# Kernel tuning notes

Hardware: AMD Instinct MI355X
Metric: run time of the kernel (lower is better)

Reference implementation:

```python
import jax, jax.numpy as jnp
import numpy as np


def setup_inputs() -> dict:
    key = jax.random.key(0)
    ks = jax.random.split(key, 12)
    N, D = 150000, 100          # user_num + news_num nodes, emb_dim
    T, E, S = 16, 262144, 4096  # timesteps, edges/step, seeds/step
    CAT, K = 20, 9
    return {
        "node_emb": jax.random.normal(ks[0], (N, D), jnp.float32),
        "cx": jax.random.normal(ks[1], (N, D), jnp.float32),
        "rel_emb": jax.random.normal(ks[2], (CAT, D), jnp.float32),
        "W_ih": jax.random.normal(ks[3], (4 * D, D), jnp.float32) * 0.1,
        "W_hh": jax.random.normal(ks[4], (4 * D, D), jnp.float32) * 0.1,
        "b_ih": jax.random.normal(ks[5], (4 * D,), jnp.float32) * 0.1,
        "b_hh": jax.random.normal(ks[6], (4 * D,), jnp.float32) * 0.1,
        "src": jax.random.randint(ks[7], (T, E), 0, N, jnp.int64),
        "dst": jax.random.randint(ks[8], (T, E), 0, N, jnp.int64),
        "cat": jax.random.randint(ks[9], (T, E), 0, CAT, jnp.int64),
        "seeds": jax.random.randint(ks[10], (T, S), 0, 100000, jnp.int64),
        "cand_idx": jax.random.randint(ks[11], (T * S, K), 0, N, jnp.int64),
    }


def reference(node_emb, cx, rel_emb, W_ih, W_hh, b_ih, b_hh,
              src, dst, cat, seeds, cand_idx):
    N, D = node_emb.shape

    def step(carry, inputs):
        emb, c = carry
        s, d, ct, seed = inputs
        # previous hidden/cell state of seed users (before aggregation)
        h_prev = emb[seed]            # [S, D]
        c_prev = c[seed]              # [S, D]
        # edge-weighted gather-multiply-mean aggregation (send_and_recv)
        msg = emb[s] * rel_emb[ct]    # [E, D]
        agg = jax.ops.segment_sum(msg, d, num_segments=N)          # [N, D]
        cnt = jax.ops.segment_sum(jnp.ones(d.shape, emb.dtype), d,
                                  num_segments=N)                  # [N]
        emb = emb + agg / jnp.maximum(cnt, 1.0)[:, None]           # residual add
        # LSTMCell update on seed users
        x = emb[seed]                                              # [S, D]
        gates = x @ W_ih.T + b_ih + h_prev @ W_hh.T + b_hh         # [S, 4D]
        i_g, f_g, g_g, o_g = jnp.split(gates, 4, axis=-1)
        c_new = jax.nn.sigmoid(f_g) * c_prev + jax.nn.sigmoid(i_g) * jnp.tanh(g_g)
        h_new = jax.nn.sigmoid(o_g) * jnp.tanh(c_new)
        emb = emb.at[seed].set(h_new)
        c = c.at[seed].set(c_new)
        return (emb, c), h_new

    (emb_final, _), seed_embs = jax.lax.scan(
        step, (node_emb, cx), (src, dst, cat, seeds))
    # seed_embs: [T, S, D] -> per-click user embeddings
    user = seed_embs.reshape(-1, D)           # [T*S, D]
    cand = emb_final[cand_idx]                # [T*S, K, D]
    scores = jnp.einsum('nd,nkd->nk', user, cand)
    return scores
```

## Files before the change

### kernel.cpp

```cpp
#include <hip/hip_runtime.h>
#include <math.h>

#define N_NODES 150000
#define NODE_STRIDE 150016
#define DIM 100
#define D4 25
#define T_STEPS 16
#define E_EDGES 262144
#define S_SEEDS 4096
#define K_CAND 9
#define SPB 16
#define NPB 8

#define CB 32
#define BSPAN 4688

__device__ __forceinline__ float sigmoidf_(float x) {
    return 1.0f / (1.0f + __expf(-x));
}


__global__ __launch_bounds__(256) void coarse_hist(
    const int* __restrict__ dst, int* __restrict__ ccnt) {
    int t = blockIdx.x >> 10;
    int i = blockIdx.x * 256 + threadIdx.x;
    __shared__ int h[CB];
    if (threadIdx.x < CB) h[threadIdx.x] = 0;
    __syncthreads();
    int d = dst[i];
    atomicAdd(&h[d / BSPAN], 1);
    __syncthreads();
    if (threadIdx.x < CB)
        atomicAdd(&ccnt[t * CB + threadIdx.x], h[threadIdx.x]);
}

__global__ __launch_bounds__(64) void coarse_scan(
    const int* __restrict__ ccnt, int* __restrict__ coffs,
    int* __restrict__ ccur) {
    int t = blockIdx.x;
    int tid = threadIdx.x;
    __shared__ int sh[CB];
    if (tid < CB) sh[tid] = ccnt[t * CB + tid];
    __syncthreads();
    if (tid == 0) {
        int run = 0;
        for (int b = 0; b < CB; b++) { int c = sh[b]; sh[b] = run; run += c; }
    }
    __syncthreads();
    if (tid < CB) {
        coffs[t * (CB + 1) + tid] = sh[tid];
        ccur[t * CB + tid] = sh[tid];
    }
    if (tid == 0) coffs[t * (CB + 1) + CB] = E_EDGES;
}

__global__ __launch_bounds__(256) void coarse_scatter(
    const int* __restrict__ src, const int* __restrict__ dst,
    const int* __restrict__ cat, int* __restrict__ ccur,
    int2* __restrict__ cbuf) {
    int t = blockIdx.x >> 10;
    int i = blockIdx.x * 256 + threadIdx.x;
    __shared__ int h[CB];
    __shared__ int base[CB];
    if (threadIdx.x < CB) h[threadIdx.x] = 0;
    __syncthreads();
    int d = dst[i];
    int b = d / BSPAN;
    int rank = atomicAdd(&h[b], 1);
    __syncthreads();
    if (threadIdx.x < CB && h[threadIdx.x] > 0)
        base[threadIdx.x] = atomicAdd(&ccur[t * CB + threadIdx.x], h[threadIdx.x]);
    __syncthreads();
    int2 entry;
    entry.x = src[i] | (cat[i] << 18);
    entry.y = d;
    cbuf[(size_t)t * E_EDGES + base[b] + rank] = entry;
}

__global__ __launch_bounds__(256) void fine_build(
    const int2* __restrict__ cbuf, const int* __restrict__ coffs,
    int4* __restrict__ meta, int* __restrict__ sorted) {
    int t = blockIdx.x >> 5;
    int b = blockIdx.x & 31;
    int node0 = b * BSPAN;
    int nodes = min(BSPAN, N_NODES - node0);
    int ebeg = coffs[t * (CB + 1) + b];
    int eend = coffs[t * (CB + 1) + b + 1];
    const int2* ebuf = cbuf + (size_t)t * E_EDGES;
    int4* mt = meta + (size_t)t * NODE_STRIDE;
    int* srt = sorted + (size_t)t * E_EDGES;
    __shared__ int cnt[BSPAN];
    __shared__ int begs[BSPAN];
    __shared__ int sums[256];
    int tid = threadIdx.x;

    for (int j = tid; j < BSPAN; j += 256) cnt[j] = 0;
    __syncthreads();
    for (int e = ebeg + tid; e < eend; e += 256)
        atomicAdd(&cnt[ebuf[e].y - node0], 1);
    __syncthreads();

    const int chunk = (BSPAN + 255) / 256;
    int cbeg = tid * chunk;
    int cend = min(cbeg + chunk, BSPAN);
    int s = 0;
    for (int j = cbeg; j < cend; j++) s += cnt[j];
    sums[tid] = s;
    __syncthreads();
    for (int d = 1; d < 256; d <<= 1) {
        int v = (tid >= d) ? sums[tid - d] : 0;
        __syncthreads();
        sums[tid] += v;
        __syncthreads();
    }
    int run = (tid == 0) ? 0 : sums[tid - 1];
    for (int j = cbeg; j < cend; j++) {
        int c = cnt[j];
        begs[j] = run;
        cnt[j] = run;
        run += c;
    }
    __syncthreads();

    for (int e = ebeg + tid; e < eend; e += 256) {
        int2 en = ebuf[e];
        int pos = atomicAdd(&cnt[en.y - node0], 1);
        srt[ebeg + pos] = en.x;
    }
    __syncthreads();

    for (int j = tid; j < nodes; j += 256) {
        int lbeg = begs[j];
        int deg = cnt[j] - lbeg;
        int gbeg = ebeg + lbeg;
        int4 m;
        m.x = deg;
        m.y = gbeg;
        m.z = (deg > 0) ? srt[gbeg] : 0;
        m.w = (deg > 1) ? srt[gbeg + 1] : 0;
        mt[node0 + j] = m;
    }
}

__global__ __launch_bounds__(256) void fused_agg(
    const float* __restrict__ emb_in, float* __restrict__ emb_out,
    const float* __restrict__ rel_emb, const int4* __restrict__ meta,
    const int* __restrict__ sorted) {
    int g = threadIdx.x >> 5;
    int lane = threadIdx.x & 31;
    int node = blockIdx.x * NPB + g;
    if (node >= N_NODES) return;
    bool act = lane < D4;
    int4 m = meta[node];
    int deg = m.x;
    float4 own = act ? ((const float4*)(emb_in + (size_t)node * DIM))[lane]
                     : make_float4(0.f, 0.f, 0.f, 0.f);
    float4 acc = make_float4(0.f, 0.f, 0.f, 0.f);
    if (deg > 0 && act) {
        float4 m0 = ((const float4*)(emb_in + (size_t)(m.z & 0x3FFFF) * DIM))[lane];
        float4 r0 = ((const float4*)(rel_emb + (size_t)(m.z >> 18) * DIM))[lane];
        float4 m1, r1;
        if (deg > 1) {
            m1 = ((const float4*)(emb_in + (size_t)(m.w & 0x3FFFF) * DIM))[lane];
            r1 = ((const float4*)(rel_emb + (size_t)(m.w >> 18) * DIM))[lane];
        }
        acc.x += m0.x * r0.x; acc.y += m0.y * r0.y;
        acc.z += m0.z * r0.z; acc.w += m0.w * r0.w;
        if (deg > 1) {
            acc.x += m1.x * r1.x; acc.y += m1.y * r1.y;
            acc.z += m1.z * r1.z; acc.w += m1.w * r1.w;
        }
    }
    for (int e = m.y + 2; e < m.y + deg; e++) {
        int p = sorted[e];
        if (act) {
            float4 mm = ((const float4*)(emb_in + (size_t)(p & 0x3FFFF) * DIM))[lane];
            float4 rr = ((const float4*)(rel_emb + (size_t)(p >> 18) * DIM))[lane];
            acc.x += mm.x * rr.x; acc.y += mm.y * rr.y;
            acc.z += mm.z * rr.z; acc.w += mm.w * rr.w;
        }
    }
    if (act) {
        float inv = (deg > 0) ? 1.0f / (float)deg : 0.0f;
        own.x += acc.x * inv; own.y += acc.y * inv;
        own.z += acc.z * inv; own.w += acc.w * inv;
        ((float4*)(emb_out + (size_t)node * DIM))[lane] = own;
    }
}

__global__ __launch_bounds__(512) void lstm_kernel(
    const float* __restrict__ emb_new, const float* __restrict__ emb_old,
    const float* __restrict__ c_state, const int* __restrict__ seeds,
    const float* __restrict__ W_ih, const float* __restrict__ W_hh,
    const float* __restrict__ b_ih, const float* __restrict__ b_hh,
    float* __restrict__ h_out, float* __restrict__ c_out) {
    __shared__ __align__(16) float xs[SPB][DIM];
    __shared__ __align__(16) float hs[SPB][DIM];
    __shared__ float gates[SPB][4 * DIM];
    int tid = threadIdx.x;
    int base = blockIdx.x * SPB;

    for (int idx = tid; idx < SPB * DIM; idx += 512) {
        int s = idx / DIM, d = idx - s * DIM;
        int node = seeds[base + s];
        xs[s][d] = emb_new[(size_t)node * DIM + d];
        hs[s][d] = emb_old[(size_t)node * DIM + d];
    }
    __syncthreads();

    if (tid < 4 * DIM) {
        int j = tid;
        float acc[SPB];
#pragma unroll
        for (int s = 0; s < SPB; s++) acc[s] = 0.0f;
        const float4* wi = (const float4*)(W_ih + (size_t)j * DIM);
        const float4* wh = (const float4*)(W_hh + (size_t)j * DIM);
        for (int dc = 0; dc < D4; dc++) {
            float4 a = wi[dc], b = wh[dc];
#pragma unroll
            for (int s = 0; s < SPB; s++) {
                float4 x = ((const float4*)xs[s])[dc];
                float4 h = ((const float4*)hs[s])[dc];
                acc[s] += x.x * a.x + x.y * a.y + x.z * a.z + x.w * a.w
                        + h.x * b.x + h.y * b.y + h.z * b.z + h.w * b.w;
            }
        }
        float bb = b_ih[j] + b_hh[j];
#pragma unroll
        for (int s = 0; s < SPB; s++) gates[s][j] = acc[s] + bb;
    }
    __syncthreads();

    for (int idx = tid; idx < SPB * DIM; idx += 512) {
        int s = idx / DIM, d = idx - s * DIM;
        int node = seeds[base + s];
        float ig = gates[s][d];
        float fg = gates[s][DIM + d];
        float gg = gates[s][2 * DIM + d];
        float og = gates[s][3 * DIM + d];
        float cp = c_state[(size_t)node * DIM + d];
        float cn = sigmoidf_(fg) * cp + sigmoidf_(ig) * tanhf(gg);
        float hn = sigmoidf_(og) * tanhf(cn);
        h_out[(size_t)(base + s) * DIM + d] = hn;
        c_out[(size_t)(base + s) * DIM + d] = cn;
    }
}

__global__ __launch_bounds__(256) void scatter_seed(
    float* __restrict__ emb, float* __restrict__ c_state,
    const int* __restrict__ seeds,
    const float* __restrict__ h_new, const float* __restrict__ c_new) {
    int i = blockIdx.x * blockDim.x + threadIdx.x;
    int sd = i / D4, q = i - sd * D4;
    int node = seeds[sd];
    ((float4*)(emb + (size_t)node * DIM))[q] =
        ((const float4*)(h_new + (size_t)sd * DIM))[q];
    ((float4*)(c_state + (size_t)node * DIM))[q] =
        ((const float4*)(c_new + (size_t)sd * DIM))[q];
}

__global__ __launch_bounds__(64) void score_kernel(
    const float* __restrict__ seed_h, const float* __restrict__ emb,
    const int* __restrict__ cand_idx, float* __restrict__ out) {
    int n = blockIdx.x;
    int lane = threadIdx.x;
    float u0 = seed_h[(size_t)n * DIM + lane];
    float u1 = (lane + 64 < DIM) ? seed_h[(size_t)n * DIM + lane + 64] : 0.0f;
    for (int k = 0; k < K_CAND; k++) {
        int node = cand_idx[n * K_CAND + k];
        const float* ce = emb + (size_t)node * DIM;
        float p = u0 * ce[lane];
        if (lane + 64 < DIM) p += u1 * ce[lane + 64];
        for (int off = 32; off > 0; off >>= 1) p += __shfl_down(p, off);
        if (lane == 0) out[n * K_CAND + k] = p;
    }
}

extern "C" void kernel_launch(void* const* d_in, const int* in_sizes, int n_in,
                              void* d_out, int out_size, void* d_ws, size_t ws_size,
                              hipStream_t stream) {
    const float* node_emb = (const float*)d_in[0];
    const float* cx       = (const float*)d_in[1];
    const float* rel_emb  = (const float*)d_in[2];
    const float* W_ih     = (const float*)d_in[3];
    const float* W_hh     = (const float*)d_in[4];
    const float* b_ih     = (const float*)d_in[5];
    const float* b_hh     = (const float*)d_in[6];
    const int*   src      = (const int*)d_in[7];
    const int*   dst      = (const int*)d_in[8];
    const int*   cat      = (const int*)d_in[9];
    const int*   seeds    = (const int*)d_in[10];
    const int*   cand     = (const int*)d_in[11];
    float* out = (float*)d_out;

    char* wsb = (char*)d_ws;
    float* emb_a = (float*)wsb; wsb += sizeof(float) * (size_t)N_NODES * DIM;
    float* emb_b = (float*)wsb; wsb += sizeof(float) * (size_t)N_NODES * DIM;
    float* cst   = (float*)wsb; wsb += sizeof(float) * (size_t)N_NODES * DIM;
    float* cnew  = (float*)wsb; wsb += sizeof(float) * (size_t)S_SEEDS * DIM;
    float* seedh = (float*)wsb; wsb += sizeof(float) * (size_t)T_STEPS * S_SEEDS * DIM;
    int4* meta   = (int4*)wsb; wsb += sizeof(int4) * (size_t)T_STEPS * NODE_STRIDE;
    int* sorted  = (int*)wsb; wsb += sizeof(int) * (size_t)T_STEPS * E_EDGES;
    int* ccnt    = (int*)wsb; wsb += sizeof(int) * T_STEPS * CB;
    int* ccur    = (int*)wsb; wsb += sizeof(int) * T_STEPS * CB;
    int* coffs   = (int*)wsb; wsb += sizeof(int) * T_STEPS * (CB + 1);
    int2* cbuf = (int2*)emb_b;

    hipMemsetAsync(ccnt, 0, sizeof(int) * T_STEPS * CB, stream);
    coarse_hist<<<T_STEPS * 1024, 256, 0, stream>>>(dst, ccnt);
    coarse_scan<<<T_STEPS, 64, 0, stream>>>(ccnt, coffs, ccur);
    coarse_scatter<<<T_STEPS * 1024, 256, 0, stream>>>(src, dst, cat, ccur, cbuf);
    fine_build<<<T_STEPS * CB, 256, 0, stream>>>(cbuf, coffs, meta, sorted);

    hipMemcpyAsync(emb_a, node_emb, sizeof(float) * (size_t)N_NODES * DIM,
                   hipMemcpyDeviceToDevice, stream);
    hipMemcpyAsync(cst, cx, sizeof(float) * (size_t)N_NODES * DIM,
                   hipMemcpyDeviceToDevice, stream);

    float* cur = emb_a;
    float* nxt = emb_b;
    for (int t = 0; t < T_STEPS; t++) {
        fused_agg<<<(N_NODES + NPB - 1) / NPB, 256, 0, stream>>>(
            cur, nxt, rel_emb,
            meta + (size_t)t * NODE_STRIDE, sorted + (size_t)t * E_EDGES);
        lstm_kernel<<<S_SEEDS / SPB, 512, 0, stream>>>(
            nxt, cur, cst, seeds + (size_t)t * S_SEEDS,
            W_ih, W_hh, b_ih, b_hh,
            seedh + (size_t)t * S_SEEDS * DIM, cnew);
        scatter_seed<<<(S_SEEDS * D4) / 256, 256, 0, stream>>>(
            nxt, cst, seeds + (size_t)t * S_SEEDS,
            seedh + (size_t)t * S_SEEDS * DIM, cnew);
        float* tmp = cur; cur = nxt; nxt = tmp;
    }
    score_kernel<<<T_STEPS * S_SEEDS, 64, 0, stream>>>(seedh, cur, cand, out);
}
```

Baseline: 1.690 ms.

## Use per-block histograms for edge bucketing, inline third neighbor, skip embedding copy

Coarse edge bucketing now computes per-block histograms and scans them, replacing global atomic cursors, with 64 buckets and 8 edges per thread. Node metadata packs degree and begin offset into one word so a third neighbor index can be stored inline, avoiding a dependent load from the sorted array for low-degree nodes. The initial device copy of node_emb is removed by reading the input directly at step 0 and alternating output buffers. This adds a serial per-column scan and depends on degrees fitting in 13 bits.

```diff
diff --git a/kernel.cpp b/kernel.cpp
--- a/kernel.cpp
+++ b/kernel.cpp
@@ -12,8 +12,11 @@
 #define SPB 16
 #define NPB 8
 
-#define CB 32
-#define BSPAN 4688
+#define CB 64
+#define BSPAN 2344
+#define EPT 8
+#define EPB (256 * EPT)
+#define CBLK (E_EDGES / EPB)
 
 __device__ __forceinline__ float sigmoidf_(float x) {
     return 1.0f / (1.0f + __expf(-x));
@@ -21,67 +24,85 @@
 
 
 __global__ __launch_bounds__(256) void coarse_hist(
-    const int* __restrict__ dst, int* __restrict__ ccnt) {
-    int t = blockIdx.x >> 10;
-    int i = blockIdx.x * 256 + threadIdx.x;
+    const int* __restrict__ dst, int* __restrict__ bh) {
+    int t = blockIdx.x / CBLK;
+    int blk = blockIdx.x % CBLK;
+    int base = t * E_EDGES + blk * EPB;
+    int tid = threadIdx.x;
     __shared__ int h[CB];
-    if (threadIdx.x < CB) h[threadIdx.x] = 0;
-    __syncthreads();
-    int d = dst[i];
-    atomicAdd(&h[d / BSPAN], 1);
-    __syncthreads();
-    if (threadIdx.x < CB)
-        atomicAdd(&ccnt[t * CB + threadIdx.x], h[threadIdx.x]);
-}
-
-__global__ __launch_bounds__(64) void coarse_scan(
-    const int* __restrict__ ccnt, int* __restrict__ coffs,
-    int* __restrict__ ccur) {
+    if (tid < CB) h[tid] = 0;
+    __syncthreads();
+#pragma unroll
+    for (int e = 0; e < EPT; e++) {
+        int d = dst[base + e * 256 + tid];
+        atomicAdd(&h[d / BSPAN], 1);
+    }
+    __syncthreads();
+    if (tid < CB) bh[(t * CBLK + blk) * CB + tid] = h[tid];
+}
+
+__global__ __launch_bounds__(64) void scan_bh(
+    int* __restrict__ bh, int* __restrict__ coffs) {
     int t = blockIdx.x;
-    int tid = threadIdx.x;
-    __shared__ int sh[CB];
-    if (tid < CB) sh[tid] = ccnt[t * CB + tid];
-    __syncthreads();
-    if (tid == 0) {
-        int run = 0;
-        for (int b = 0; b < CB; b++) { int c = sh[b]; sh[b] = run; run += c; }
-    }
-    __syncthreads();
-    if (tid < CB) {
-        coffs[t * (CB + 1) + tid] = sh[tid];
-        ccur[t * CB + tid] = sh[tid];
-    }
-    if (tid == 0) coffs[t * (CB + 1) + CB] = E_EDGES;
+    int b = threadIdx.x;
+    int run = 0;
+    for (int blk = 0; blk < CBLK; blk++) {
+        int idx = (t * CBLK + blk) * CB + b;
+        int v = bh[idx];
+        bh[idx] = run;
+        run += v;
+    }
+    __shared__ int tot[CB];
+    tot[b] = run;
+    __syncthreads();
+    if (b == 0) {
+        int r = 0;
+        for (int i = 0; i < CB; i++) { int c = tot[i]; tot[i] = r; r += c; }
+    }
+    __syncthreads();
+    coffs[t * (CB + 1) + b] = tot[b];
+    if (b == 0) coffs[t * (CB + 1) + CB] = E_EDGES;
 }
 
 __global__ __launch_bounds__(256) void coarse_scatter(
     const int* __restrict__ src, const int* __restrict__ dst,
-    const int* __restrict__ cat, int* __restrict__ ccur,
-    int2* __restrict__ cbuf) {
-    int t = blockIdx.x >> 10;
-    int i = blockIdx.x * 256 + threadIdx.x;
+    const int* __restrict__ cat, const int* __restrict__ bh,
+    const int* __restrict__ coffs, int2* __restrict__ cbuf) {
+    int t = blockIdx.x / CBLK;
+    int blk = blockIdx.x % CBLK;
+    int base = t * E_EDGES + blk * EPB;
+    int tid = threadIdx.x;
     __shared__ int h[CB];
-    __shared__ int base[CB];
-    if (threadIdx.x < CB) h[threadIdx.x] = 0;
-    __syncthreads();
-    int d = dst[i];
-    int b = d / BSPAN;
-    int rank = atomicAdd(&h[b], 1);
-    __syncthreads();
-    if (threadIdx.x < CB && h[threadIdx.x] > 0)
-        base[threadIdx.x] = atomicAdd(&ccur[t * CB + threadIdx.x], h[threadIdx.x]);
-    __syncthreads();
-    int2 entry;
-    entry.x = src[i] | (cat[i] << 18);
-    entry.y = d;
-    cbuf[(size_t)t * E_EDGES + base[b] + rank] = entry;
+    __shared__ int gbase[CB];
+    if (tid < CB) h[tid] = 0;
+    __syncthreads();
+    int rank[EPT], bb[EPT], dd[EPT];
+#pragma unroll
+    for (int e = 0; e < EPT; e++) {
+        int d = dst[base + e * 256 + tid];
+        int b = d / BSPAN;
+        dd[e] = d; bb[e] = b;
+        rank[e] = atomicAdd(&h[b], 1);
+    }
+    __syncthreads();
+    if (tid < CB)
+        gbase[tid] = coffs[t * (CB + 1) + tid] + bh[(t * CBLK + blk) * CB + tid];
+    __syncthreads();
+#pragma unroll
+    for (int e = 0; e < EPT; e++) {
+        int i = base + e * 256 + tid;
+        int2 en;
+        en.x = src[i] | (cat[i] << 18);
+        en.y = dd[e];
+        cbuf[(size_t)t * E_EDGES + gbase[bb[e]] + rank[e]] = en;
+    }
 }
 
 __global__ __launch_bounds__(256) void fine_build(
     const int2* __restrict__ cbuf, const int* __restrict__ coffs,
     int4* __restrict__ meta, int* __restrict__ sorted) {
-    int t = blockIdx.x >> 5;
-    int b = blockIdx.x & 31;
+    int t = blockIdx.x >> 6;
+    int b = blockIdx.x & 63;
     int node0 = b * BSPAN;
     int nodes = min(BSPAN, N_NODES - node0);
     int ebeg = coffs[t * (CB + 1) + b];
@@ -134,10 +155,10 @@
         int deg = cnt[j] - lbeg;
         int gbeg = ebeg + lbeg;
         int4 m;
-        m.x = deg;
-        m.y = gbeg;
-        m.z = (deg > 0) ? srt[gbeg] : 0;
-        m.w = (deg > 1) ? srt[gbeg + 1] : 0;
+        m.x = gbeg | (deg << 19);
+        m.y = (deg > 0) ? srt[gbeg] : 0;
+        m.z = (deg > 1) ? srt[gbeg + 1] : 0;
+        m.w = (deg > 2) ? srt[gbeg + 2] : 0;
         mt[node0 + j] = m;
     }
 }
@@ -151,27 +172,33 @@
     int node = blockIdx.x * NPB + g;
     if (node >= N_NODES) return;
     bool act = lane < D4;
-    int4 m = meta[node];
-    int deg = m.x;
     float4 own = act ? ((const float4*)(emb_in + (size_t)node * DIM))[lane]
                      : make_float4(0.f, 0.f, 0.f, 0.f);
+    int4 m = meta[node];
+    int deg = ((unsigned)m.x) >> 19;
+    int beg = m.x & 0x7FFFF;
     float4 acc = make_float4(0.f, 0.f, 0.f, 0.f);
-    if (deg > 0 && act) {
-        float4 m0 = ((const float4*)(emb_in + (size_t)(m.z & 0x3FFFF) * DIM))[lane];
-        float4 r0 = ((const float4*)(rel_emb + (size_t)(m.z >> 18) * DIM))[lane];
-        float4 m1, r1;
+    if (act) {
+        if (deg > 0) {
+            float4 mm = ((const float4*)(emb_in + (size_t)(m.y & 0x3FFFF) * DIM))[lane];
+            float4 rr = ((const float4*)(rel_emb + (size_t)(m.y >> 18) * DIM))[lane];
+            acc.x += mm.x * rr.x; acc.y += mm.y * rr.y;
+            acc.z += mm.z * rr.z; acc.w += mm.w * rr.w;
+        }
         if (deg > 1) {
-            m1 = ((const float4*)(emb_in + (size_t)(m.w & 0x3FFFF) * DIM))[lane];
-            r1 = ((const float4*)(rel_emb + (size_t)(m.w >> 18) * DIM))[lane];
-        }
-        acc.x += m0.x * r0.x; acc.y += m0.y * r0.y;
-        acc.z += m0.z * r0.z; acc.w += m0.w * r0.w;
-        if (deg > 1) {
-            acc.x += m1.x * r1.x; acc.y += m1.y * r1.y;
-            acc.z += m1.z * r1.z; acc.w += m1.w * r1.w;
-        }
-    }
-    for (int e = m.y + 2; e < m.y + deg; e++) {
+            float4 mm = ((const float4*)(emb_in + (size_t)(m.z & 0x3FFFF) * DIM))[lane];
+            float4 rr = ((const float4*)(rel_emb + (size_t)(m.z >> 18) * DIM))[lane];
+            acc.x += mm.x * rr.x; acc.y += mm.y * rr.y;
+            acc.z += mm.z * rr.z; acc.w += mm.w * rr.w;
+        }
+        if (deg > 2) {
+            float4 mm = ((const float4*)(emb_in + (size_t)(m.w & 0x3FFFF) * DIM))[lane];
+            float4 rr = ((const float4*)(rel_emb + (size_t)(m.w >> 18) * DIM))[lane];
+            acc.x += mm.x * rr.x; acc.y += mm.y * rr.y;
+            acc.z += mm.z * rr.z; acc.w += mm.w * rr.w;
+        }
+    }
+    for (int e = beg + 3; e < beg + deg; e++) {
         int p = sorted[e];
         if (act) {
             float4 mm = ((const float4*)(emb_in + (size_t)(p & 0x3FFFF) * DIM))[lane];
@@ -301,25 +328,23 @@
     float* seedh = (float*)wsb; wsb += sizeof(float) * (size_t)T_STEPS * S_SEEDS * DIM;
     int4* meta   = (int4*)wsb; wsb += sizeof(int4) * (size_t)T_STEPS * NODE_STRIDE;
     int* sorted  = (int*)wsb; wsb += sizeof(int) * (size_t)T_STEPS * E_EDGES;
-    int* ccnt    = (int*)wsb; wsb += sizeof(int) * T_STEPS * CB;
-    int* ccur    = (int*)wsb; wsb += sizeof(int) * T_STEPS * CB;
+    int* bh      = (int*)wsb; wsb += sizeof(int) * (size_t)T_STEPS * CBLK * CB;
     int* coffs   = (int*)wsb; wsb += sizeof(int) * T_STEPS * (CB + 1);
     int2* cbuf = (int2*)emb_b;
 
-    hipMemsetAsync(ccnt, 0, sizeof(int) * T_STEPS * CB, stream);
-    coarse_hist<<<T_STEPS * 1024, 256, 0, stream>>>(dst, ccnt);
-    coarse_scan<<<T_STEPS, 64, 0, stream>>>(ccnt, coffs, ccur);
-    coarse_scatter<<<T_STEPS * 1024, 256, 0, stream>>>(src, dst, cat, ccur, cbuf);
+    coarse_hist<<<T_STEPS * CBLK, 256, 0, stream>>>(dst, bh);
+    scan_bh<<<T_STEPS, 64, 0, stream>>>(bh, coffs);
+    coarse_scatter<<<T_STEPS * CBLK, 256, 0, stream>>>(
+        src, dst, cat, bh, coffs, cbuf);
     fine_build<<<T_STEPS * CB, 256, 0, stream>>>(cbuf, coffs, meta, sorted);
 
-    hipMemcpyAsync(emb_a, node_emb, sizeof(float) * (size_t)N_NODES * DIM,
-                   hipMemcpyDeviceToDevice, stream);
     hipMemcpyAsync(cst, cx, sizeof(float) * (size_t)N_NODES * DIM,
                    hipMemcpyDeviceToDevice, stream);
 
-    float* cur = emb_a;
-    float* nxt = emb_b;
+    const float* cur = node_emb;
+    float* bufs[2] = {emb_b, emb_a};
     for (int t = 0; t < T_STEPS; t++) {
+        float* nxt = bufs[t & 1];
         fused_agg<<<(N_NODES + NPB - 1) / NPB, 256, 0, stream>>>(
             cur, nxt, rel_emb,
             meta + (size_t)t * NODE_STRIDE, sorted + (size_t)t * E_EDGES);
@@ -330,7 +355,7 @@
         scatter_seed<<<(S_SEEDS * D4) / 256, 256, 0, stream>>>(
             nxt, cst, seeds + (size_t)t * S_SEEDS,
             seedh + (size_t)t * S_SEEDS * DIM, cnew);
-        float* tmp = cur; cur = nxt; nxt = tmp;
+        cur = nxt;
     }
     score_kernel<<<T_STEPS * S_SEEDS, 64, 0, stream>>>(seedh, cur, cand, out);
 }
```

After: 1.543 ms. 8.7% less time.
